# Kernel optimization log

Measured on AMD Instinct MI355X. Metric: run time of the kernel, lower is better.

## Reference

```python
import jax, jax.numpy as jnp
import numpy as np

B = 32; C = 3; IMG = 224; P = 16; G = IMG // P  # 14x14 patches
N = G * G + 1  # 197 tokens incl cls
D = 768; L = 12; H = 12; HD = D // H; FF = 4 * D
NR = (2 * G - 1) * (2 * G - 1) + 3  # 732
SCALE = HD ** -0.5


def _rel_index():
    ch = np.arange(G); cw = np.arange(G)
    coords = np.stack(np.meshgrid(ch, cw, indexing='ij')).reshape(2, -1)
    rel = (coords[:, :, None] - coords[:, None, :]).transpose(1, 2, 0).copy()
    rel[:, :, 0] += G - 1
    rel[:, :, 1] += G - 1
    rel[:, :, 0] *= 2 * G - 1
    idx = np.zeros((N, N), dtype=np.int32)
    idx[1:, 1:] = rel.sum(-1)
    idx[0, :] = NR - 3
    idx[:, 0] = NR - 2
    idx[0, 0] = NR - 1
    return jnp.asarray(idx)


def setup_inputs() -> dict:
    key = jax.random.key(0)
    ks = jax.random.split(key, 10)
    def nrm(k, shape, s=0.02):
        return jax.random.normal(k, shape, jnp.float32) * s
    return {
        'x': jax.random.normal(ks[0], (B, C, IMG, IMG), jnp.float32),
        'patch_w': nrm(ks[1], (D, C, P, P)),
        'patch_b': jnp.zeros((D,), jnp.float32),
        'cls_token': nrm(ks[2], (1, 1, D)),
        'ln1_g': jnp.ones((L, D), jnp.float32), 'ln1_b': jnp.zeros((L, D), jnp.float32),
        'qkv_w': nrm(ks[3], (L, 3 * D, D)),
        'q_bias': jnp.zeros((L, D), jnp.float32), 'v_bias': jnp.zeros((L, D), jnp.float32),
        'rel_table': nrm(ks[4], (L, NR, H)),
        'proj_w': nrm(ks[5], (L, D, D)), 'proj_b': jnp.zeros((L, D), jnp.float32),
        'gamma1': 0.1 * jnp.ones((L, D), jnp.float32),
        'ln2_g': jnp.ones((L, D), jnp.float32), 'ln2_b': jnp.zeros((L, D), jnp.float32),
        'fc1_w': nrm(ks[6], (L, FF, D)), 'fc1_b': jnp.zeros((L, FF), jnp.float32),
        'fc2_w': nrm(ks[7], (L, D, FF)), 'fc2_b': jnp.zeros((L, D), jnp.float32),
        'gamma2': 0.1 * jnp.ones((L, D), jnp.float32),
        'fcn_g': jnp.ones((D,), jnp.float32), 'fcn_b': jnp.zeros((D,), jnp.float32),
        'rel_index': _rel_index(),
    }


def _ln(x, g, b):
    m = x.mean(-1, keepdims=True)
    v = ((x - m) ** 2).mean(-1, keepdims=True)
    return (x - m) * jax.lax.rsqrt(v + 1e-5) * g + b


def reference(x, patch_w, patch_b, cls_token, ln1_g, ln1_b, qkv_w, q_bias, v_bias,
              rel_table, proj_w, proj_b, gamma1, ln2_g, ln2_b, fc1_w, fc1_b,
              fc2_w, fc2_b, gamma2, fcn_g, fcn_b, rel_index):
    b = x.shape[0]
    # patch embed: stride-P conv == unfold + matmul
    xp = x.reshape(b, C, G, P, G, P).transpose(0, 2, 4, 1, 3, 5).reshape(b, G * G, C * P * P)
    tok = xp @ patch_w.reshape(D, C * P * P).T + patch_b  # [B, 196, D]
    tok = jnp.concatenate([jnp.broadcast_to(cls_token, (b, 1, D)), tok], axis=1)  # [B, N, D]

    def block(t, p):
        g1, b1, qw, qb, vb, rt, pw, pb, gm1, g2, b2, f1w, f1b, f2w, f2b, gm2 = p
        h = _ln(t, g1, b1)
        qkv_bias = jnp.concatenate([qb, jnp.zeros_like(qb), vb])
        qkv = (h @ qw.T + qkv_bias).reshape(b, N, 3, H, HD).transpose(2, 0, 3, 1, 4)
        q, k, v = qkv[0] * SCALE, qkv[1], qkv[2]  # [B,H,N,HD]
        rpb = jnp.transpose(rt[rel_index], (2, 0, 1))  # [H,N,N]
        attn = jax.nn.softmax(jnp.einsum('bhid,bhjd->bhij', q, k) + rpb[None], axis=-1)
        o = jnp.einsum('bhij,bhjd->bhid', attn, v).transpose(0, 2, 1, 3).reshape(b, N, D)
        t = t + gm1 * (o @ pw.T + pb)
        h2 = _ln(t, g2, b2)
        m = jax.nn.gelu(h2 @ f1w.T + f1b, approximate=False) @ f2w.T + f2b
        return t + gm2 * m, None

    params = (ln1_g, ln1_b, qkv_w, q_bias, v_bias, rel_table, proj_w, proj_b,
              gamma1, ln2_g, ln2_b, fc1_w, fc1_b, fc2_w, fc2_b, gamma2)
    tok, _ = jax.lax.scan(block, tok, params)
    # BEiT-style mean pooling over patch tokens + fc_norm
    return _ln(tok[:, 1:].mean(axis=1), fcn_g, fcn_b)  # [B, D]
```

## Files before the change

### kernel.cpp

```cpp
#include <hip/hip_runtime.h>


#define BATCH 32
#define NTOK 197
#define NLAYER 12
#define NRR 732
#define MROWS (BATCH * NTOK)
#define MPAD 6400

#define NKV 224
#define QT_N 13
#define VSTR 232
#define PSTR 232
#define RPB_PER_LH (QT_N * 14 * 4 * 16 * 4)
#define RPB_PER_L (RPB_PER_LH * 12)
#define WL_ELEMS 8257536

typedef __attribute__((ext_vector_type(8))) short bf16x8_t;
typedef __attribute__((ext_vector_type(4))) float f32x4_t;

__device__ __forceinline__ unsigned short f2bf_rn(float f) {
  unsigned u = __float_as_uint(f);
  unsigned r = (u + 0x7FFFu + ((u >> 16) & 1u)) >> 16;
  return (unsigned short)r;
}
__device__ __forceinline__ float bf2f(unsigned short u) {
  return __uint_as_float(((unsigned)u) << 16);
}

__device__ __forceinline__ void gld16(const unsigned short* g, unsigned short* l) {
  __builtin_amdgcn_global_load_lds(
      (const __attribute__((address_space(1))) unsigned int*)g,
      (__attribute__((address_space(3))) unsigned int*)l, 16, 0, 0);
}

__global__ void cvt4(const float4* __restrict__ s, ushort4* __restrict__ d, int n4) {
  int i = blockIdx.x * 256 + threadIdx.x;
  if (i >= n4) return;
  float4 v = s[i];
  ushort4 r;
  r.x = f2bf_rn(v.x); r.y = f2bf_rn(v.y); r.z = f2bf_rn(v.z); r.w = f2bf_rn(v.w);
  d[i] = r;
}

__global__ void cvt_layer(const float4* __restrict__ qw, const float4* __restrict__ pw,
                          const float4* __restrict__ f1, const float4* __restrict__ f2,
                          ushort4* __restrict__ dst) {
  const int n_q = 2304 * 768 / 4;
  const int n_p = 768 * 768 / 4;
  const int n_1 = 3072 * 768 / 4;
  int i = blockIdx.x * 256 + threadIdx.x;
  float4 v;
  if (i < n_q) v = qw[i];
  else if (i < n_q + n_p) v = pw[i - n_q];
  else if (i < n_q + n_p + n_1) v = f1[i - n_q - n_p];
  else if (i < n_q + n_p + 2 * n_1) v = f2[i - n_q - n_p - n_1];
  else return;
  ushort4 r;
  r.x = f2bf_rn(v.x); r.y = f2bf_rn(v.y); r.z = f2bf_rn(v.z); r.w = f2bf_rn(v.w);
  dst[i] = r;
}

__global__ void build_rpb(const float* __restrict__ rt, const int* __restrict__ ridx,
                          unsigned short* __restrict__ dst) {
  int idx = blockIdx.x * 256 + threadIdx.x;
  if (idx >= RPB_PER_L * NLAYER) return;
  int r = idx & 3;
  int fr = (idx >> 2) & 15;
  int fq = (idx >> 6) & 3;
  int t2 = idx >> 8;
  int jt = t2 % 14; t2 /= 14;
  int qt = t2 % QT_N; t2 /= QT_N;
  int h = t2 % 12;
  int l = t2 / 12;
  int row = qt * 16 + fq * 4 + r;
  int col = jt * 16 + fr;
  float v = -30000.f;
  if (row < 197 && col < 197)
    v = rt[((size_t)l * NRR + ridx[row * 197 + col]) * 12 + h];
  dst[idx] = f2bf_rn(v);
}

__global__ void build_xp(const float* __restrict__ x, unsigned short* __restrict__ xp) {
  int idx = blockIdx.x * 256 + threadIdx.x;
  if (idx >= 6272 * 768) return;
  int r = idx / 768, c = idx - r * 768;
  int b = r / 196, p = r - b * 196;
  int gy = p / 14, gx = p - gy * 14;
  int ch = c >> 8, rem = c & 255, py = rem >> 4, px = rem & 15;
  float v = x[(((size_t)b * 3 + ch) * 224 + gy * 16 + py) * 224 + gx * 16 + px];
  xp[(size_t)(b * 197 + 1 + p) * 768 + c] = f2bf_rn(v);
}

__global__ void fill_cls(const float* __restrict__ cls, float* __restrict__ tok) {
  int idx = blockIdx.x * 256 + threadIdx.x;
  int b = idx / 768, d = idx - b * 768;
  tok[(size_t)(b * 197) * 768 + d] = cls[d];
}

__global__ __launch_bounds__(256) void ln_rows(const float* __restrict__ x,
                                               unsigned short* __restrict__ y,
                                               const float* __restrict__ g,
                                               const float* __restrict__ b) {
  int row = blockIdx.x;
  const float* xr = x + (size_t)row * 768;
  int t = threadIdx.x;
  float v0 = xr[t], v1 = xr[t + 256], v2 = xr[t + 512];
  float s = v0 + v1 + v2;
  float q = v0 * v0 + v1 * v1 + v2 * v2;
  for (int off = 32; off; off >>= 1) { s += __shfl_xor(s, off); q += __shfl_xor(q, off); }
  __shared__ float rs[4], rq[4];
  int wave = t >> 6;
  if ((t & 63) == 0) { rs[wave] = s; rq[wave] = q; }
  __syncthreads();
  s = rs[0] + rs[1] + rs[2] + rs[3];
  q = rq[0] + rq[1] + rq[2] + rq[3];
  float mean = s * (1.f / 768.f);
  float var = q * (1.f / 768.f) - mean * mean;
  float rstd = rsqrtf(var + 1e-5f);
  unsigned short* yr = y + (size_t)row * 768;
  yr[t]       = f2bf_rn((v0 - mean) * rstd * g[t]       + b[t]);
  yr[t + 256] = f2bf_rn((v1 - mean) * rstd * g[t + 256] + b[t + 256]);
  yr[t + 512] = f2bf_rn((v2 - mean) * rstd * g[t + 512] + b[t + 512]);
}

template <int MODE, int BM>
__global__ __launch_bounds__(256, (BM == 64 ? 3 : 2)) void gemm_t(
    const unsigned short* __restrict__ A, const unsigned short* __restrict__ Bw,
    float* __restrict__ Cf, unsigned short* __restrict__ Cb,
    const float* __restrict__ bias, const float* __restrict__ bias2,
    const float* __restrict__ gamma, int K, int N, int nbx) {
  constexpr int MI = BM / 32;
  __shared__ __align__(16) unsigned short As[2][BM * 64];
  __shared__ __align__(16) unsigned short Bs[2][128 * 64];
  const int tid = threadIdx.x;
  const int wave = tid >> 6, lane = tid & 63;

  const int nwg = gridDim.x;
  const int q8 = nwg >> 3, r8 = nwg & 7;
  const int xcd = blockIdx.x & 7, ii = blockIdx.x >> 3;
  const int wg = (xcd < r8 ? xcd * (q8 + 1) : r8 * (q8 + 1) + (xcd - r8) * q8) + ii;
  const int m0 = (wg / nbx) * BM, n0 = (wg % nbx) * 128;

  const int wm = (wave & 1) * (MI * 16), wn = (wave >> 1) * 64;
  f32x4_t acc[MI][4] = {};
  const int srow = lane >> 2;
  const int scol = ((lane & 3) ^ ((lane >> 3) & 3)) * 8;
  const unsigned short* Abase = A + (size_t)(m0 + srow) * K + scol;
  const unsigned short* Bbase = Bw + (size_t)(n0 + srow) * K + scol;
  const int fr = lane & 15, fq = lane >> 4;
  const int rchunk = (fq ^ ((fr >> 1) & 3)) * 8;

  auto stage = [&](int buf, int k0) {
#pragma unroll
    for (int s = 0; s < 2; ++s) {
#pragma unroll
      for (int u0 = 0; u0 < BM / 64; ++u0) {
        int u = wave + u0 * 4;
        gld16(Abase + (size_t)(u * 16) * K + k0 + s * 32, &As[buf][s * (BM * 32) + u * 512]);
      }
#pragma unroll
      for (int u0 = 0; u0 < 2; ++u0) {
        int u = wave + u0 * 4;
        gld16(Bbase + (size_t)(u * 16) * K + k0 + s * 32, &Bs[buf][s * 4096 + u * 512]);
      }
    }
  };

  stage(0, 0);
  asm volatile("s_waitcnt vmcnt(0)" ::: "memory");
  __builtin_amdgcn_s_barrier();

  const int nk = K >> 6;
  for (int t = 0; t < nk; ++t) {
    const int buf = t & 1;
    if (t + 1 < nk) stage(buf ^ 1, (t + 1) << 6);
#pragma unroll
    for (int s = 0; s < 2; ++s) {
      bf16x8_t af[MI], bfr[4];
#pragma unroll
      for (int i = 0; i < MI; ++i)
        af[i] = *(const bf16x8_t*)(&As[buf][s * (BM * 32) + (wm + i * 16 + fr) * 32 + rchunk]);
#pragma unroll
      for (int j = 0; j < 4; ++j)
        bfr[j] = *(const bf16x8_t*)(&Bs[buf][s * 4096 + (wn + j * 16 + fr) * 32 + rchunk]);
#pragma unroll
      for (int i = 0; i < MI; ++i)
#pragma unroll
        for (int j = 0; j < 4; ++j)
          acc[i][j] = __builtin_amdgcn_mfma_f32_16x16x32_bf16(af[i], bfr[j], acc[i][j], 0, 0, 0);
    }
    asm volatile("s_waitcnt vmcnt(0)" ::: "memory");
    __builtin_amdgcn_s_barrier();
  }

  const int er = (lane >> 4) * 4;
  const int ec = lane & 15;
#pragma unroll
  for (int i = 0; i < MI; ++i) {
#pragma unroll
    for (int j = 0; j < 4; ++j) {
#pragma unroll
      for (int r = 0; r < 4; ++r) {
        int row = m0 + wm + i * 16 + er + r;
        int col = n0 + wn + j * 16 + ec;
        float v = acc[i][j][r];
        size_t idx = (size_t)row * N + col;
        if constexpr (MODE == 0) {
          Cf[idx] = v + bias[col];
        } else if constexpr (MODE == 1) {
          float bv = (col < 768) ? bias[col] : (col >= 1536 ? bias2[col - 1536] : 0.f);
          v += bv;
          if (col < 768) v *= 0.125f;
          Cb[idx] = f2bf_rn(v);
        } else if constexpr (MODE == 2) {
          Cf[idx] = Cf[idx] + gamma[col] * (v + bias[col]);
        } else {
          float tt = v + bias[col];
          float gv = 0.5f * tt * (1.f + erff(tt * 0.70710678118654752f));
          Cb[idx] = f2bf_rn(gv);
        }
      }
    }
  }
}

__global__ __launch_bounds__(256) void attn_mfma(
    const unsigned short* __restrict__ qkv,
    const unsigned short* __restrict__ rpb,
    unsigned short* __restrict__ o) {
  const int bh = blockIdx.x;
  const int b = bh / 12, h = bh - b * 12;
  __shared__ __align__(16) unsigned short Vt[64 * VSTR];
  __shared__ __align__(16) unsigned short Pls[4][16 * PSTR];
  const int t = threadIdx.x;
  const int wave = t >> 6, lane = t & 63;
  const int fr = lane & 15, fq = lane >> 4;
  const size_t qbase = (size_t)(b * 197) * 2304 + h * 64;
  const unsigned short* rph = rpb + (size_t)h * RPB_PER_LH;

  for (int idx = t; idx < NKV * 16; idx += 256) {
    int j = idx >> 4, d0 = (idx & 15) * 4;
    ushort4 v = *(const ushort4*)(qkv + qbase + 1536 + (size_t)j * 2304 + d0);
    Vt[(d0 + 0) * VSTR + j] = v.x;
    Vt[(d0 + 1) * VSTR + j] = v.y;
    Vt[(d0 + 2) * VSTR + j] = v.z;
    Vt[(d0 + 3) * VSTR + j] = v.w;
  }
  __syncthreads();

  unsigned short* P = &Pls[wave][0];
  for (int qt = wave; qt < QT_N; qt += 4) {
    const unsigned short* qrow = qkv + qbase + (size_t)(qt * 16 + fr) * 2304 + fq * 8;
    bf16x8_t qa0 = *(const bf16x8_t*)(qrow);
    bf16x8_t qa1 = *(const bf16x8_t*)(qrow + 32);
    f32x4_t S[14];
#pragma unroll
    for (int jt = 0; jt < 14; ++jt) {
      const unsigned short* krow = qkv + qbase + 768 + (size_t)(jt * 16 + fr) * 2304 + fq * 8;
      bf16x8_t kb0 = *(const bf16x8_t*)(krow);
      bf16x8_t kb1 = *(const bf16x8_t*)(krow + 32);
      f32x4_t s = {};
      s = __builtin_amdgcn_mfma_f32_16x16x32_bf16(qa0, kb0, s, 0, 0, 0);
      s = __builtin_amdgcn_mfma_f32_16x16x32_bf16(qa1, kb1, s, 0, 0, 0);
      ushort4 rb = *(const ushort4*)(rph + ((size_t)(qt * 14 + jt) * 4 + fq) * 64 + fr * 4);
      s[0] += bf2f(rb.x); s[1] += bf2f(rb.y); s[2] += bf2f(rb.z); s[3] += bf2f(rb.w);
      S[jt] = s;
    }
    float mx[4], sum[4];
#pragma unroll
    for (int r = 0; r < 4; ++r) mx[r] = S[0][r];
#pragma unroll
    for (int jt = 1; jt < 14; ++jt)
#pragma unroll
      for (int r = 0; r < 4; ++r) mx[r] = fmaxf(mx[r], S[jt][r]);
#pragma unroll
    for (int r = 0; r < 4; ++r) {
      for (int off = 1; off < 16; off <<= 1) mx[r] = fmaxf(mx[r], __shfl_xor(mx[r], off));
      sum[r] = 0.f;
    }
#pragma unroll
    for (int jt = 0; jt < 14; ++jt) {
#pragma unroll
      for (int r = 0; r < 4; ++r) {
        float p = __expf(S[jt][r] - mx[r]);
        sum[r] += p;
        P[(fq * 4 + r) * PSTR + jt * 16 + fr] = f2bf_rn(p);
      }
    }
    float rinv[4];
#pragma unroll
    for (int r = 0; r < 4; ++r) {
      for (int off = 1; off < 16; off <<= 1) sum[r] += __shfl_xor(sum[r], off);
      rinv[r] = 1.f / sum[r];
    }
    bf16x8_t pa[7];
#pragma unroll
    for (int ks = 0; ks < 7; ++ks)
      pa[ks] = *(const bf16x8_t*)(P + fr * PSTR + ks * 32 + fq * 8);
#pragma unroll
    for (int nt = 0; nt < 4; ++nt) {
      f32x4_t O = {};
#pragma unroll
      for (int ks = 0; ks < 7; ++ks) {
        bf16x8_t vb = *(const bf16x8_t*)(Vt + (nt * 16 + fr) * VSTR + ks * 32 + fq * 8);
        O = __builtin_amdgcn_mfma_f32_16x16x32_bf16(pa[ks], vb, O, 0, 0, 0);
      }
#pragma unroll
      for (int r = 0; r < 4; ++r) {
        int row = qt * 16 + fq * 4 + r;
        if (row < 197)
          o[(size_t)(b * 197 + row) * 768 + h * 64 + nt * 16 + fr] = f2bf_rn(O[r] * rinv[r]);
      }
    }
  }
}

__global__ __launch_bounds__(256) void pool_ln(const float* __restrict__ tok,
                                               const float* __restrict__ g,
                                               const float* __restrict__ bb,
                                               float* __restrict__ out) {
  int b = blockIdx.x;
  __shared__ float pool[768];
  int t = threadIdx.x;
  for (int c = t; c < 768; c += 256) {
    float s = 0.f;
    const float* p = tok + (size_t)(b * 197 + 1) * 768 + c;
    for (int i = 0; i < 196; ++i) s += p[(size_t)i * 768];
    pool[c] = s * (1.f / 196.f);
  }
  __syncthreads();
  float s = 0.f, q = 0.f;
  for (int c = t; c < 768; c += 256) { float v = pool[c]; s += v; q += v * v; }
  for (int off = 32; off; off >>= 1) { s += __shfl_xor(s, off); q += __shfl_xor(q, off); }
  __shared__ float rs[4], rq[4];
  if ((t & 63) == 0) { rs[t >> 6] = s; rq[t >> 6] = q; }
  __syncthreads();
  s = rs[0] + rs[1] + rs[2] + rs[3];
  q = rq[0] + rq[1] + rq[2] + rq[3];
  float mean = s * (1.f / 768.f);
  float var = q * (1.f / 768.f) - mean * mean;
  float rstd = rsqrtf(var + 1e-5f);
  for (int c = t; c < 768; c += 256)
    out[(size_t)b * 768 + c] = (pool[c] - mean) * rstd * g[c] + bb[c];
}

extern "C" void kernel_launch(void* const* d_in, const int* in_sizes, int n_in,
                              void* d_out, int out_size, void* d_ws, size_t ws_size,
                              hipStream_t stream) {
  const float* x         = (const float*)d_in[0];
  const float* patch_w   = (const float*)d_in[1];
  const float* patch_b   = (const float*)d_in[2];
  const float* cls_tok   = (const float*)d_in[3];
  const float* ln1_g     = (const float*)d_in[4];
  const float* ln1_b     = (const float*)d_in[5];
  const float* qkv_w     = (const float*)d_in[6];
  const float* q_bias    = (const float*)d_in[7];
  const float* v_bias    = (const float*)d_in[8];
  const float* rel_table = (const float*)d_in[9];
  const float* proj_w    = (const float*)d_in[10];
  const float* proj_b    = (const float*)d_in[11];
  const float* gamma1    = (const float*)d_in[12];
  const float* ln2_g     = (const float*)d_in[13];
  const float* ln2_b     = (const float*)d_in[14];
  const float* fc1_w     = (const float*)d_in[15];
  const float* fc1_b     = (const float*)d_in[16];
  const float* fc2_w     = (const float*)d_in[17];
  const float* fc2_b     = (const float*)d_in[18];
  const float* gamma2    = (const float*)d_in[19];
  const float* fcn_g     = (const float*)d_in[20];
  const float* fcn_b     = (const float*)d_in[21];
  const int* rel_index   = (const int*)d_in[22];
  float* out = (float*)d_out;

  char* ws = (char*)d_ws;
  size_t off = 0;
  auto take = [&](size_t bytes) {
    char* p = ws + off;
    off += (bytes + 255) & ~(size_t)255;
    return p;
  };
  unsigned short* wl     = (unsigned short*)take((size_t)WL_ELEMS * 2);
  unsigned short* pwb    = (unsigned short*)take((size_t)589824 * 2);
  float*          tokf   = (float*)take((size_t)MPAD * 768 * 4);
  unsigned short* hb     = (unsigned short*)take((size_t)MPAD * 768 * 2);
  unsigned short* qkvb   = (unsigned short*)take((size_t)MPAD * 2304 * 2);
  unsigned short* ffb    = (unsigned short*)take((size_t)MPAD * 3072 * 2);
  unsigned short* rpbAll = (unsigned short*)take((size_t)RPB_PER_L * NLAYER * 2);
  unsigned short* xp = ffb;
  unsigned short* ob = hb;
  unsigned short* wl_qkv = wl;
  unsigned short* wl_proj = wl + (size_t)2304 * 768;
  unsigned short* wl_fc1 = wl_proj + (size_t)768 * 768;
  unsigned short* wl_fc2 = wl_fc1 + (size_t)3072 * 768;

  build_rpb<<<(RPB_PER_L * NLAYER + 255) / 256, 256, 0, stream>>>(rel_table, rel_index, rpbAll);

  cvt4<<<576, 256, 0, stream>>>((const float4*)patch_w, (ushort4*)pwb, 147456);
  build_xp<<<18816, 256, 0, stream>>>(x, xp);
  gemm_t<0, 64><<<600, 256, 0, stream>>>(xp, pwb, tokf, nullptr, patch_b,
                                         nullptr, nullptr, 768, 768, 6);
  fill_cls<<<96, 256, 0, stream>>>(cls_tok, tokf);

  for (int l = 0; l < NLAYER; ++l) {
    cvt_layer<<<(WL_ELEMS / 4 + 255) / 256, 256, 0, stream>>>(
        (const float4*)(qkv_w + (size_t)l * 2304 * 768),
        (const float4*)(proj_w + (size_t)l * 768 * 768),
        (const float4*)(fc1_w + (size_t)l * 3072 * 768),
        (const float4*)(fc2_w + (size_t)l * 768 * 3072), (ushort4*)wl);
    ln_rows<<<MROWS, 256, 0, stream>>>(tokf, hb, ln1_g + l * 768, ln1_b + l * 768);
    gemm_t<1, 128><<<900, 256, 0, stream>>>(hb, wl_qkv, nullptr, qkvb,
                                            q_bias + l * 768, v_bias + l * 768,
                                            nullptr, 768, 2304, 18);
    attn_mfma<<<384, 256, 0, stream>>>(qkvb, rpbAll + (size_t)l * RPB_PER_L, ob);
    gemm_t<2, 64><<<600, 256, 0, stream>>>(ob, wl_proj, tokf, nullptr,
                                           proj_b + l * 768, nullptr,
                                           gamma1 + l * 768, 768, 768, 6);
    ln_rows<<<MROWS, 256, 0, stream>>>(tokf, hb, ln2_g + l * 768, ln2_b + l * 768);
    gemm_t<3, 128><<<1200, 256, 0, stream>>>(hb, wl_fc1, nullptr, ffb,
                                             fc1_b + l * 3072, nullptr, nullptr,
                                             768, 3072, 24);
    gemm_t<2, 64><<<600, 256, 0, stream>>>(ffb, wl_fc2, tokf, nullptr,
                                           fc2_b + l * 768, nullptr,
                                           gamma2 + l * 768, 3072, 768, 6);
  }
  pool_ln<<<32, 256, 0, stream>>>(tokf, fcn_g, fcn_b, out);
}
```

Before: 3.433 ms.

## Switch GEMM to three-stage LDS ring with 32-wide K steps and partial waits

```diff
diff --git a/kernel.cpp b/kernel.cpp
--- a/kernel.cpp
+++ b/kernel.cpp
@@ -125,14 +125,16 @@
 }
 
 template <int MODE, int BM>
-__global__ __launch_bounds__(256, (BM == 64 ? 3 : 2)) void gemm_t(
+__global__ __launch_bounds__(256, (BM == 64 ? 4 : 3)) void gemm_t(
     const unsigned short* __restrict__ A, const unsigned short* __restrict__ Bw,
     float* __restrict__ Cf, unsigned short* __restrict__ Cb,
     const float* __restrict__ bias, const float* __restrict__ bias2,
     const float* __restrict__ gamma, int K, int N, int nbx) {
   constexpr int MI = BM / 32;
-  __shared__ __align__(16) unsigned short As[2][BM * 64];
-  __shared__ __align__(16) unsigned short Bs[2][128 * 64];
+  constexpr int AG = BM / 64;
+  constexpr int LPS = AG + 2;
+  __shared__ __align__(16) unsigned short As[3][BM * 32];
+  __shared__ __align__(16) unsigned short Bs[3][128 * 32];
   const int tid = threadIdx.x;
   const int wave = tid >> 6, lane = tid & 63;
 
@@ -151,47 +153,51 @@
   const int fr = lane & 15, fq = lane >> 4;
   const int rchunk = (fq ^ ((fr >> 1) & 3)) * 8;
 
-  auto stage = [&](int buf, int k0) {
-#pragma unroll
-    for (int s = 0; s < 2; ++s) {
-#pragma unroll
-      for (int u0 = 0; u0 < BM / 64; ++u0) {
-        int u = wave + u0 * 4;
-        gld16(Abase + (size_t)(u * 16) * K + k0 + s * 32, &As[buf][s * (BM * 32) + u * 512]);
-      }
-#pragma unroll
-      for (int u0 = 0; u0 < 2; ++u0) {
-        int u = wave + u0 * 4;
-        gld16(Bbase + (size_t)(u * 16) * K + k0 + s * 32, &Bs[buf][s * 4096 + u * 512]);
-      }
+  auto stage = [&](int slot, int k0) {
+#pragma unroll
+    for (int u0 = 0; u0 < AG; ++u0) {
+      int u = wave + u0 * 4;
+      gld16(Abase + (size_t)(u * 16) * K + k0, &As[slot][u * 512]);
+    }
+#pragma unroll
+    for (int u0 = 0; u0 < 2; ++u0) {
+      int u = wave + u0 * 4;
+      gld16(Bbase + (size_t)(u * 16) * K + k0, &Bs[slot][u * 512]);
     }
   };
 
+  const int nk = K >> 5;
   stage(0, 0);
-  asm volatile("s_waitcnt vmcnt(0)" ::: "memory");
-  __builtin_amdgcn_s_barrier();
-
-  const int nk = K >> 6;
+  stage(1, 32);
+
+  int cur = 0;
   for (int t = 0; t < nk; ++t) {
-    const int buf = t & 1;
-    if (t + 1 < nk) stage(buf ^ 1, (t + 1) << 6);
-#pragma unroll
-    for (int s = 0; s < 2; ++s) {
+    if (t + 1 < nk) {
+      if constexpr (LPS == 3) asm volatile("s_waitcnt vmcnt(3)" ::: "memory");
+      else                    asm volatile("s_waitcnt vmcnt(4)" ::: "memory");
+    } else {
+      asm volatile("s_waitcnt vmcnt(0)" ::: "memory");
+    }
+    asm volatile("s_barrier" ::: "memory");
+    if (t + 2 < nk) {
+      int s2 = cur + 2; if (s2 >= 3) s2 -= 3;
+      stage(s2, (t + 2) << 5);
+    }
+    {
       bf16x8_t af[MI], bfr[4];
 #pragma unroll
       for (int i = 0; i < MI; ++i)
-        af[i] = *(const bf16x8_t*)(&As[buf][s * (BM * 32) + (wm + i * 16 + fr) * 32 + rchunk]);
+        af[i] = *(const bf16x8_t*)(&As[cur][(wm + i * 16 + fr) * 32 + rchunk]);
 #pragma unroll
       for (int j = 0; j < 4; ++j)
-        bfr[j] = *(const bf16x8_t*)(&Bs[buf][s * 4096 + (wn + j * 16 + fr) * 32 + rchunk]);
+        bfr[j] = *(const bf16x8_t*)(&Bs[cur][(wn + j * 16 + fr) * 32 + rchunk]);
 #pragma unroll
       for (int i = 0; i < MI; ++i)
 #pragma unroll
         for (int j = 0; j < 4; ++j)
           acc[i][j] = __builtin_amdgcn_mfma_f32_16x16x32_bf16(af[i], bfr[j], acc[i][j], 0, 0, 0);
     }
-    asm volatile("s_waitcnt vmcnt(0)" ::: "memory");
-    __builtin_amdgcn_s_barrier();
+    ++cur; if (cur == 3) cur = 0;
   }
 
   const int er = (lane >> 4) * 4;
```

After: 3.475 ms. Within noise of the previous version (+1.2%).

## Triple-buffer GEMM LDS pipeline with 32-wide K steps and one barrier per step

Applied to the files above, without the earlier changes.

```diff
diff --git a/kernel.cpp b/kernel.cpp
--- a/kernel.cpp
+++ b/kernel.cpp
@@ -125,14 +125,20 @@
 }
 
 template <int MODE, int BM>
-__global__ __launch_bounds__(256, (BM == 64 ? 3 : 2)) void gemm_t(
+__global__ __launch_bounds__(256, (BM == 64 ? 4 : 3)) void gemm_t(
     const unsigned short* __restrict__ A, const unsigned short* __restrict__ Bw,
     float* __restrict__ Cf, unsigned short* __restrict__ Cb,
     const float* __restrict__ bias, const float* __restrict__ bias2,
     const float* __restrict__ gamma, int K, int N, int nbx) {
   constexpr int MI = BM / 32;
-  __shared__ __align__(16) unsigned short As[2][BM * 64];
-  __shared__ __align__(16) unsigned short Bs[2][128 * 64];
+  constexpr int AG = BM / 64;
+  constexpr int LPS = AG + 2;
+  __shared__ __align__(16) unsigned short As0[BM * 32];
+  __shared__ __align__(16) unsigned short As1[BM * 32];
+  __shared__ __align__(16) unsigned short As2[BM * 32];
+  __shared__ __align__(16) unsigned short Bs0[128 * 32];
+  __shared__ __align__(16) unsigned short Bs1[128 * 32];
+  __shared__ __align__(16) unsigned short Bs2[128 * 32];
   const int tid = threadIdx.x;
   const int wave = tid >> 6, lane = tid & 63;
 
@@ -146,52 +152,65 @@
   f32x4_t acc[MI][4] = {};
   const int srow = lane >> 2;
   const int scol = ((lane & 3) ^ ((lane >> 3) & 3)) * 8;
-  const unsigned short* Abase = A + (size_t)(m0 + srow) * K + scol;
-  const unsigned short* Bbase = Bw + (size_t)(n0 + srow) * K + scol;
   const int fr = lane & 15, fq = lane >> 4;
   const int rchunk = (fq ^ ((fr >> 1) & 3)) * 8;
 
-  auto stage = [&](int buf, int k0) {
-#pragma unroll
-    for (int s = 0; s < 2; ++s) {
-#pragma unroll
-      for (int u0 = 0; u0 < BM / 64; ++u0) {
-        int u = wave + u0 * 4;
-        gld16(Abase + (size_t)(u * 16) * K + k0 + s * 32, &As[buf][s * (BM * 32) + u * 512]);
-      }
-#pragma unroll
-      for (int u0 = 0; u0 < 2; ++u0) {
-        int u = wave + u0 * 4;
-        gld16(Bbase + (size_t)(u * 16) * K + k0 + s * 32, &Bs[buf][s * 4096 + u * 512]);
-      }
-    }
+  const unsigned short* pa[AG];
+  const unsigned short* pb[2];
+#pragma unroll
+  for (int u0 = 0; u0 < AG; ++u0)
+    pa[u0] = A + (size_t)(m0 + (wave + u0 * 4) * 16 + srow) * K + scol;
+#pragma unroll
+  for (int u0 = 0; u0 < 2; ++u0)
+    pb[u0] = Bw + (size_t)(n0 + (wave + u0 * 4) * 16 + srow) * K + scol;
+
+  auto stage = [&](unsigned short* Asl, unsigned short* Bsl, int k0) {
+#pragma unroll
+    for (int u0 = 0; u0 < AG; ++u0)
+      gld16(pa[u0] + k0, Asl + (wave + u0 * 4) * 512);
+#pragma unroll
+    for (int u0 = 0; u0 < 2; ++u0)
+      gld16(pb[u0] + k0, Bsl + (wave + u0 * 4) * 512);
   };
 
-  stage(0, 0);
-  asm volatile("s_waitcnt vmcnt(0)" ::: "memory");
-  __builtin_amdgcn_s_barrier();
-
-  const int nk = K >> 6;
-  for (int t = 0; t < nk; ++t) {
-    const int buf = t & 1;
-    if (t + 1 < nk) stage(buf ^ 1, (t + 1) << 6);
-#pragma unroll
-    for (int s = 0; s < 2; ++s) {
-      bf16x8_t af[MI], bfr[4];
-#pragma unroll
-      for (int i = 0; i < MI; ++i)
-        af[i] = *(const bf16x8_t*)(&As[buf][s * (BM * 32) + (wm + i * 16 + fr) * 32 + rchunk]);
+  auto compute = [&](const unsigned short* Asl, const unsigned short* Bsl) {
+    bf16x8_t af[MI], bfr[4];
+#pragma unroll
+    for (int i = 0; i < MI; ++i)
+      af[i] = *(const bf16x8_t*)(Asl + (wm + i * 16 + fr) * 32 + rchunk);
+#pragma unroll
+    for (int j = 0; j < 4; ++j)
+      bfr[j] = *(const bf16x8_t*)(Bsl + (wn + j * 16 + fr) * 32 + rchunk);
+    __builtin_amdgcn_s_setprio(1);
+#pragma unroll
+    for (int i = 0; i < MI; ++i)
 #pragma unroll
       for (int j = 0; j < 4; ++j)
-        bfr[j] = *(const bf16x8_t*)(&Bs[buf][s * 4096 + (wn + j * 16 + fr) * 32 + rchunk]);
-#pragma unroll
-      for (int i = 0; i < MI; ++i)
-#pragma unroll
-        for (int j = 0; j < 4; ++j)
-          acc[i][j] = __builtin_amdgcn_mfma_f32_16x16x32_bf16(af[i], bfr[j], acc[i][j], 0, 0, 0);
-    }
-    asm volatile("s_waitcnt vmcnt(0)" ::: "memory");
+        acc[i][j] = __builtin_amdgcn_mfma_f32_16x16x32_bf16(af[i], bfr[j], acc[i][j], 0, 0, 0);
+    __builtin_amdgcn_s_setprio(0);
+  };
+
+  auto waitN = [&]() {
+    if constexpr (LPS == 3) asm volatile("s_waitcnt vmcnt(3)" ::: "memory");
+    else                    asm volatile("s_waitcnt vmcnt(4)" ::: "memory");
+  };
+  auto wait0 = [&]() { asm volatile("s_waitcnt vmcnt(0)" ::: "memory"); };
+
+  const int nk = K >> 5;
+  stage(As0, Bs0, 0);
+  for (int t0 = 0; t0 < nk; t0 += 3) {
+    if (t0 + 1 < nk) { stage(As1, Bs1, (t0 + 1) << 5); waitN(); }
+    else             { wait0(); }
     __builtin_amdgcn_s_barrier();
+    compute(As0, Bs0);
+    if (t0 + 2 < nk) { stage(As2, Bs2, (t0 + 2) << 5); waitN(); }
+    else             { wait0(); }
+    __builtin_amdgcn_s_barrier();
+    compute(As1, Bs1);
+    if (t0 + 3 < nk) { stage(As0, Bs0, (t0 + 3) << 5); waitN(); }
+    else             { wait0(); }
+    __builtin_amdgcn_s_barrier();
+    compute(As2, Bs2);
   }
 
   const int er = (lane >> 4) * 4;
```

Result: faster. 3.336 ms (-2.8%).
